# Kernel optimization log

Measured on AMD Instinct MI355X. Metric: run time of the kernel, lower is better.

## Reference

```python
import jax, jax.numpy as jnp
import numpy as np

NUM_MEL = 80
STACK_FRAMES = 4   # encoder.embed.right_context + 1
STRIDE = 4         # encoder.embed.subsampling_rate
N_SUB = 1          # n_subsequent
NCB = 1            # num_codebooks
EMB_DIM = 16
NUM_EMB = 8192
ENC_DIM = 512
B, T = 16, 2048
T_ENC = (T - STACK_FRAMES) // STRIDE + 1  # 512
EPS_LN = 1e-6


def setup_inputs() -> dict:
    key = jax.random.key(0)
    k = jax.random.split(key, 6)
    feats = jax.random.normal(k[0], (B, T, NUM_MEL), dtype=jnp.float32)
    feats_lengths = jax.random.randint(k[1], (B,), T // 2, T + 1, dtype=jnp.int32)
    encoder_out = jax.random.normal(k[2], (B, T_ENC, ENC_DIM), dtype=jnp.float32)
    in_dim = NUM_MEL * STRIDE
    lim = float(np.sqrt(6.0 / (in_dim + EMB_DIM * NCB)))  # xavier-uniform
    projection = jax.random.uniform(k[3], (in_dim, EMB_DIM * NCB), jnp.float32, -lim, lim)
    emb = jax.random.normal(k[4], (NUM_EMB, NCB, EMB_DIM), dtype=jnp.float32)
    embeddings = emb / (jnp.linalg.norm(emb, axis=-1, keepdims=True) + 1e-8)
    top_n_out = 0.02 * jax.random.normal(k[5], (N_SUB, NCB, ENC_DIM, NUM_EMB), dtype=jnp.float32)
    return {"feats": feats, "feats_lengths": feats_lengths, "encoder_out": encoder_out,
            "projection": projection, "embeddings": embeddings, "top_n_out": top_n_out}


def _stack_features(feats, lens):
    b, t, f = feats.shape
    n = (t - STACK_FRAMES) // STRIDE + 1
    idx = jnp.arange(n)[:, None] * STRIDE + jnp.arange(STACK_FRAMES)[None, :]  # [n, S]
    stack = feats[:, idx, :].reshape(b, n, STACK_FRAMES * f)                   # [B, n, S*F]
    mask = jnp.arange(t)[None, :] < lens[:, None]                              # [B, T]
    sub_mask = jnp.all(mask[:, idx], axis=-1)                                  # [B, n]
    mean = stack.mean(-1, keepdims=True)
    var = stack.var(-1, keepdims=True)
    stack = (stack - mean) * jax.lax.rsqrt(var + EPS_LN)  # LayerNorm, no affine
    return stack, sub_mask


def _nearest_idx(stack, projection, embeddings):
    x = stack @ projection                                         # [B, n, ncb*E]
    x = x / (jnp.linalg.norm(x, axis=-1, keepdims=True) + 1e-8)
    b, n, _ = x.shape
    v, ncb, e = embeddings.shape
    xf = x.reshape(b * n, ncb, e)
    dots = jnp.einsum('nce,vce->ncv', xf, embeddings)              # [N, ncb, V]
    x2 = jnp.sum(xf * xf, -1, keepdims=True)                       # [N, ncb, 1]
    e2 = jnp.sum(embeddings * embeddings, -1).T[None]              # [1, ncb, V]
    dist = x2 - 2.0 * dots + e2
    codes = jnp.argmin(dist, axis=-1)                              # [N, ncb]
    return codes.reshape(b, n, ncb)


def _forward(feats, feats_lengths, encoder_out, projection, embeddings, top_n_out):
    stack, stack_mask = _stack_features(feats, feats_lengths)
    target = _nearest_idx(stack, projection, embeddings)           # [B, n, ncb]
    tq = stack_mask.shape[1]
    # unfold(n_subsequent=1) -> [B, Tq, ns, ncb]
    target = target[:, :tq, None, :]
    # encoder output mask (subsampled lengths)
    t_enc = encoder_out.shape[1]
    out_mask = jnp.arange(t_enc)[None, :] < (feats_lengths // STRIDE)[:, None]
    logits = jnp.einsum('btd,scdv->bsctv', encoder_out, top_n_out)  # [B, ns, ncb, T', V]
    logits = logits[:, :, :, :tq, :][:, :, :, :-1, :]               # frames 0..Tq-2
    target = target[:, 1:]                                          # targets 1..Tq-1
    masks = (out_mask[:, :tq] & stack_mask)[:, 1:]                  # [B, Tq-1] bool
    mf = masks.astype(logits.dtype)
    logp = jax.nn.log_softmax(logits, axis=-1)
    tgt_bsct = jnp.transpose(target, (0, 2, 3, 1))                  # [B, ns, ncb, Tq-1]
    nll = -jnp.take_along_axis(logp, tgt_bsct[..., None], axis=-1)[..., 0]
    mfull = jnp.broadcast_to(mf[:, None, None, :], nll.shape)
    loss = (nll * mfull).sum() / mfull.sum()
    num_codes = mf.sum() * NCB
    pred = jnp.argmax(logits, axis=-1)                              # [B, ns, ncb, Tq-1]
    corr = (pred == tgt_bsct).astype(logits.dtype)
    codes_acc = (corr * mfull).sum() / num_codes
    masked_tgt = target * masks[:, :, None, None].astype(target.dtype)
    presence = jnp.zeros((NUM_EMB,), jnp.int32).at[masked_tgt.reshape(-1)].set(1)
    uniq_num_codes = presence.sum().astype(jnp.float32)
    return loss, codes_acc, num_codes, uniq_num_codes


def reference(feats, feats_lengths, encoder_out, projection, embeddings, top_n_out):
    return _forward(feats, feats_lengths, encoder_out, projection, embeddings, top_n_out)
```

## Files before the change

### kernel.cpp

```cpp
#include <hip/hip_runtime.h>
#include <math.h>

typedef __attribute__((ext_vector_type(4))) float f32x4;
typedef __attribute__((ext_vector_type(8))) short bf16x8;

#define NB 16
#define NT 2048
#define NMEL 80
#define NPOS 512
#define EDIM 16
#define NEMB 8192
#define ENCD 512
#define MROWS (NB*511)
#define MPAD 8192
#define NVT 64

__device__ __forceinline__ unsigned short f2bf(float x) {
    union { float f; unsigned u; } v; v.f = x;
    unsigned r = v.u + 0x7fffu + ((v.u >> 16) & 1u);
    return (unsigned short)(r >> 16);
}

__device__ __forceinline__ void gl_lds16(const void* gsrc, void* lds) {
    __builtin_amdgcn_global_load_lds(
        (const __attribute__((address_space(1))) unsigned int*)gsrc,
        (__attribute__((address_space(3))) unsigned int*)lds,
        16, 0, 0);
}

__global__ __launch_bounds__(256) void prep_kernel(
    const float* __restrict__ feats, const float* __restrict__ proj,
    const float* __restrict__ emb, const float* __restrict__ enc,
    const float* __restrict__ tno,
    unsigned short* __restrict__ ynB, unsigned short* __restrict__ embB,
    float* __restrict__ h2, int* __restrict__ presence,
    unsigned char* __restrict__ encF8, unsigned char* __restrict__ tnoF8)
{
    __shared__ float tileT[32][33];
    const int bid = blockIdx.x;
    const int tid = threadIdx.x;

    if (bid < 512) {
        const int lane = tid & 63;
        const int wave = tid >> 6;
        const int gbase = bid * 16 + wave * 4;
        if (bid < 32) presence[bid * 256 + tid] = 0;

        float yn[4][EDIM];
        #pragma unroll
        for (int pi = 0; pi < 4; ++pi) {
            const int g = gbase + pi;
            const int b = g >> 9;
            const int i = g & 511;
            float xv[5];
            float s = 0.f, sq = 0.f;
            #pragma unroll
            for (int qq = 0; qq < 5; ++qq) {
                const int d = lane + 64 * qq;
                const int j = d / 80, k = d - j * 80;
                const float v = feats[((b * NT) + (i * 4 + j)) * NMEL + k];
                xv[qq] = v; s += v; sq += v * v;
            }
            for (int m = 1; m < 64; m <<= 1) { s += __shfl_xor(s, m); sq += __shfl_xor(sq, m); }
            const float mean = s * (1.0f / 320.0f);
            const float var  = sq * (1.0f / 320.0f) - mean * mean;
            const float rstd = rsqrtf(var + 1e-6f);
            float acc[EDIM];
            #pragma unroll
            for (int e = 0; e < EDIM; ++e) acc[e] = 0.f;
            #pragma unroll
            for (int qq = 0; qq < 5; ++qq) {
                const int d = lane + 64 * qq;
                const float xn = (xv[qq] - mean) * rstd;
                #pragma unroll
                for (int e = 0; e < EDIM; ++e) acc[e] += xn * proj[d * EDIM + e];
            }
            for (int m = 1; m < 64; m <<= 1) {
                #pragma unroll
                for (int e = 0; e < EDIM; ++e) acc[e] += __shfl_xor(acc[e], m);
            }
            float nsq = 0.f;
            #pragma unroll
            for (int e = 0; e < EDIM; ++e) nsq += acc[e] * acc[e];
            const float inv = 1.0f / (sqrtf(nsq) + 1e-8f);
            #pragma unroll
            for (int e = 0; e < EDIM; ++e) yn[pi][e] = acc[e] * inv;
        }
        #pragma unroll
        for (int pi = 0; pi < 4; ++pi) {
            if (lane == pi) {
                unsigned short* dst = &ynB[(size_t)(gbase + pi) * 32];
                #pragma unroll
                for (int e = 0; e < EDIM; ++e) dst[e] = f2bf(yn[pi][e]);
                #pragma unroll
                for (int e = EDIM; e < 32; ++e) dst[e] = 0;
            }
        }
    } else if (bid < 1024) {
        const int bid2 = bid - 512;
        const int lane = tid & 63;
        #pragma unroll
        for (int pass = 0; pass < 4; ++pass) {
            const int m = bid2 * 16 + pass * 4 + (tid >> 6);
            const int d = lane * 8;
            uint2 o = make_uint2(0u, 0u);
            if (m < MROWS) {
                const int b = m / 511, t = m - b * 511;
                const float4 f0 = *(const float4*)&enc[((size_t)(b * 512 + t)) * ENCD + d];
                const float4 f1 = *(const float4*)&enc[((size_t)(b * 512 + t)) * ENCD + d + 4];
                int w0 = __builtin_amdgcn_cvt_pk_fp8_f32(f0.x, f0.y, 0, false);
                w0     = __builtin_amdgcn_cvt_pk_fp8_f32(f0.z, f0.w, w0, true);
                int w1 = __builtin_amdgcn_cvt_pk_fp8_f32(f1.x, f1.y, 0, false);
                w1     = __builtin_amdgcn_cvt_pk_fp8_f32(f1.z, f1.w, w1, true);
                o.x = (unsigned)w0; o.y = (unsigned)w1;
            }
            *(uint2*)&encF8[(size_t)m * ENCD + d] = o;
        }
    } else if (bid < 2048) {
        const int bid2 = bid - 1024;
        const int tx = tid & 31, ty = tid >> 5;
        const int np = tid >> 3, kc = tid & 7;
        #pragma unroll
        for (int it = 0; it < 4; ++it) {
            const int tile = bid2 * 4 + it;
            const int n0 = (tile & 255) * 32;
            const int k0 = (tile >> 8) * 32;
            __syncthreads();
            #pragma unroll
            for (int i = 0; i < 4; ++i)
                tileT[ty + 8 * i][tx] = tno[(size_t)(k0 + ty + 8 * i) * NEMB + n0 + tx];
            __syncthreads();
            const float t0 = 16.0f * tileT[kc * 4 + 0][np];
            const float t1 = 16.0f * tileT[kc * 4 + 1][np];
            const float t2 = 16.0f * tileT[kc * 4 + 2][np];
            const float t3 = 16.0f * tileT[kc * 4 + 3][np];
            int w = __builtin_amdgcn_cvt_pk_fp8_f32(t0, t1, 0, false);
            w     = __builtin_amdgcn_cvt_pk_fp8_f32(t2, t3, w, true);
            ((unsigned*)tnoF8)[(size_t)(n0 + np) * (ENCD / 4) + (k0 >> 2) + kc] = (unsigned)w;
        }
    } else {
        const int row = (bid - 2048) * 256 + tid;
        const float* ep = &emb[(size_t)row * EDIM];
        const float4 e0 = *(const float4*)&ep[0];
        const float4 e1 = *(const float4*)&ep[4];
        const float4 e2v = *(const float4*)&ep[8];
        const float4 e3 = *(const float4*)&ep[12];
        const float e2 = e0.x*e0.x + e0.y*e0.y + e0.z*e0.z + e0.w*e0.w
                       + e1.x*e1.x + e1.y*e1.y + e1.z*e1.z + e1.w*e1.w
                       + e2v.x*e2v.x + e2v.y*e2v.y + e2v.z*e2v.z + e2v.w*e2v.w
                       + e3.x*e3.x + e3.y*e3.y + e3.z*e3.z + e3.w*e3.w;
        h2[row] = 0.5f * e2;
        unsigned short* dst = &embB[(size_t)row * 32];
        dst[0]  = f2bf(e0.x); dst[1]  = f2bf(e0.y); dst[2]  = f2bf(e0.z); dst[3]  = f2bf(e0.w);
        dst[4]  = f2bf(e1.x); dst[5]  = f2bf(e1.y); dst[6]  = f2bf(e1.z); dst[7]  = f2bf(e1.w);
        dst[8]  = f2bf(e2v.x); dst[9]  = f2bf(e2v.y); dst[10] = f2bf(e2v.z); dst[11] = f2bf(e2v.w);
        dst[12] = f2bf(e3.x); dst[13] = f2bf(e3.y); dst[14] = f2bf(e3.z); dst[15] = f2bf(e3.w);
        #pragma unroll
        for (int e = EDIM; e < 32; ++e) dst[e] = 0;
    }
}

__global__ __launch_bounds__(256) void codes_mfma(
    const unsigned short* __restrict__ ynB, const unsigned short* __restrict__ embB,
    const float* __restrict__ h2,
    float* __restrict__ pscore, int* __restrict__ pcidx)
{
    const int tid = threadIdx.x;
    const int lane = tid & 63;
    const int wave = tid >> 6;
    const int pgrp  = blockIdx.x >> 2;
    const int chunk = blockIdx.x & 3;
    const int p0 = pgrp * 64 + wave * 16;
    const int l15 = lane & 15, q = lane >> 4;

    const bf16x8 a = *(const bf16x8*)&ynB[(size_t)(p0 + l15) * 32 + q * 8];

    float mn[4]; int mi[4];
    #pragma unroll
    for (int r = 0; r < 4; ++r) { mn[r] = INFINITY; mi[r] = 0x7fffffff; }

    const int e0 = chunk * 2048;
    #pragma unroll 4
    for (int g = 0; g < 128; ++g) {
        const int eidx = e0 + g * 16 + l15;
        const bf16x8 b = *(const bf16x8*)&embB[(size_t)eidx * 32 + q * 8];
        const float hv = h2[eidx];
        f32x4 d = __builtin_amdgcn_mfma_f32_16x16x32_bf16(a, b, (f32x4){0.f, 0.f, 0.f, 0.f}, 0, 0, 0);
        #pragma unroll
        for (int r = 0; r < 4; ++r) {
            const float sc = hv - d[r];
            if (sc < mn[r]) { mn[r] = sc; mi[r] = eidx; }
        }
    }
    #pragma unroll
    for (int m = 1; m < 16; m <<= 1) {
        #pragma unroll
        for (int r = 0; r < 4; ++r) {
            const float ov = __shfl_xor(mn[r], m);
            const int   oi = __shfl_xor(mi[r], m);
            if (ov < mn[r] || (ov == mn[r] && oi < mi[r])) { mn[r] = ov; mi[r] = oi; }
        }
    }
    if (l15 == 0) {
        #pragma unroll
        for (int r = 0; r < 4; ++r) {
            pscore[chunk * MPAD + p0 + q * 4 + r] = mn[r];
            pcidx [chunk * MPAD + p0 + q * 4 + r] = mi[r];
        }
    }
}

__global__ __launch_bounds__(256) void codes_merge(
    const float* __restrict__ pscore, const int* __restrict__ pcidx,
    int* __restrict__ codes)
{
    const int g = blockIdx.x * 256 + threadIdx.x;
    float m = INFINITY; int mi = 0x7fffffff;
    #pragma unroll
    for (int c = 0; c < 4; ++c) {
        const float s = pscore[c * MPAD + g];
        const int  ix = pcidx [c * MPAD + g];
        if (s < m || (s == m && ix < mi)) { m = s; mi = ix; }
    }
    codes[g] = mi;
}

__global__ __launch_bounds__(256, 5) void logits_mfma(
    const unsigned char* __restrict__ encF8, const unsigned char* __restrict__ tnoF8,
    const int* __restrict__ codes,
    float* __restrict__ pm, float* __restrict__ ps, int* __restrict__ pidx,
    float* __restrict__ tgtlog)
{
    __shared__ __align__(16) unsigned char As3[3][128 * 32];
    __shared__ __align__(16) unsigned char Bs3[3][128 * 32];
    __shared__ float redM[2][128];
    __shared__ float redS[2][128];
    __shared__ int   redI[2][128];

    const int tid  = threadIdx.x;
    const int lane = tid & 63;
    const int wave = tid >> 6;
    const int wr = wave >> 1, wc = wave & 1;

    const int bid = blockIdx.x;
    const int xcd = bid & 7;
    const int idx = bid >> 3;
    const int mt  = xcd * 8 + (idx & 7);
    const int vt  = idx >> 3;
    const int m0 = mt * 128, n0 = vt * 128;

    const int srow = lane >> 1;
    const int gcB  = ((lane & 1) ^ ((lane >> 3) & 1)) * 16;
    const size_t abase0 = (size_t)(m0 + wave * 32 + srow) * ENCD + gcB;
    const size_t bbase0 = (size_t)(n0 + wave * 32 + srow) * ENCD + gcB;

#define STAGE(t, buf)                                                                        \
    {                                                                                        \
        const int k0s = (t) * 32;                                                            \
        gl_lds16(encF8 + abase0 + k0s, &As3[buf][(wave * 32) * 32]);                         \
        gl_lds16(tnoF8 + bbase0 + k0s, &Bs3[buf][(wave * 32) * 32]);                         \
    }

    f32x4 acc[4][4];
    #pragma unroll
    for (int i = 0; i < 4; ++i)
        #pragma unroll
        for (int j = 0; j < 4; ++j)
            acc[i][j] = (f32x4){0.f, 0.f, 0.f, 0.f};

    const int l15 = lane & 15, q = lane >> 4;
    const int rsw = (l15 >> 2) & 1;
    const int co  = (((q >> 1) ^ rsw) * 16) + (q & 1) * 8;

    STAGE(0, 0);
    STAGE(1, 1);

    #pragma unroll
    for (int t = 0; t < 16; ++t) {
        if (t < 15) { asm volatile("s_waitcnt vmcnt(2)" ::: "memory"); }
        else        { asm volatile("s_waitcnt vmcnt(0)" ::: "memory"); }
        __builtin_amdgcn_s_barrier();
        __builtin_amdgcn_sched_barrier(0);
        if (t + 2 < 16) {
            const int nb = (t + 2) % 3;
            STAGE(t + 2, nb);
        }
        const unsigned char* Ab = As3[t % 3];
        const unsigned char* Bb = Bs3[t % 3];
        long a[4], b[4];
        #pragma unroll
        for (int mi = 0; mi < 4; ++mi)
            a[mi] = *(const long*)&Ab[(wr * 64 + mi * 16 + l15) * 32 + co];
        #pragma unroll
        for (int ni = 0; ni < 4; ++ni)
            b[ni] = *(const long*)&Bb[(wc * 64 + ni * 16 + l15) * 32 + co];
        __builtin_amdgcn_s_setprio(1);
        #pragma unroll
        for (int mi = 0; mi < 4; ++mi)
            #pragma unroll
            for (int ni = 0; ni < 4; ++ni)
                acc[mi][ni] = __builtin_amdgcn_mfma_f32_16x16x32_fp8_fp8(a[mi], b[ni], acc[mi][ni], 0, 0, 0);
        __builtin_amdgcn_s_setprio(0);
    }
#undef STAGE

    #pragma unroll
    for (int mi = 0; mi < 4; ++mi)
        #pragma unroll
        for (int ni = 0; ni < 4; ++ni)
            acc[mi][ni] *= 0.0625f;

    #pragma unroll
    for (int mi = 0; mi < 4; ++mi) {
        #pragma unroll
        for (int r = 0; r < 4; ++r) {
            const int rl = wr * 64 + mi * 16 + q * 4 + r;
            float lm = -INFINITY; int li = 0;
            #pragma unroll
            for (int ni = 0; ni < 4; ++ni) {
                const float v = acc[mi][ni][r];
                const int col = wc * 64 + ni * 16 + l15;
                if (v > lm) { lm = v; li = col; }
            }
            #pragma unroll
            for (int mk = 8; mk >= 1; mk >>= 1) {
                const float ov = __shfl_xor(lm, mk);
                const int   oi = __shfl_xor(li, mk);
                if (ov > lm || (ov == lm && oi < li)) { lm = ov; li = oi; }
            }
            float le = 0.f;
            #pragma unroll
            for (int ni = 0; ni < 4; ++ni) le += __expf(acc[mi][ni][r] - lm);
            #pragma unroll
            for (int mk = 8; mk >= 1; mk >>= 1) le += __shfl_xor(le, mk);

            if (l15 == 0) { redM[wc][rl] = lm; redS[wc][rl] = le; redI[wc][rl] = li; }

            const int mg = m0 + rl;
            if (mg < MROWS) {
                const int bb = mg / 511, tt = mg - bb * 511;
                const int tv = codes[bb * NPOS + tt + 1];
                const int rel = tv - n0 - wc * 64;
                #pragma unroll
                for (int ni = 0; ni < 4; ++ni) {
                    if (rel >= ni * 16 && rel < ni * 16 + 16 && (rel & 15) == l15)
                        tgtlog[mg] = acc[mi][ni][r];
                }
            }
        }
    }
    __syncthreads();
    if (tid < 128) {
        const int rl = tid;
        const int mg = m0 + rl;
        if (mg < MROWS) {
            const float mA = redM[0][rl], mB = redM[1][rl];
            const int   iA = redI[0][rl], iB = redI[1][rl];
            float gm; int gi;
            if (mB > mA || (mB == mA && iB + 64 < iA)) { gm = mB; gi = 64 + iB; } else { gm = mA; gi = iA; }
            const float S = redS[0][rl] * __expf(mA - gm) + redS[1][rl] * __expf(mB - gm);
            pm[(size_t)vt * MPAD + mg]   = gm;
            ps[(size_t)vt * MPAD + mg]   = S;
            pidx[(size_t)vt * MPAD + mg] = n0 + gi;
        }
    }
}

__global__ __launch_bounds__(256) void combine_kernel(
    const float* __restrict__ pm, const float* __restrict__ ps,
    const int* __restrict__ pidx, const float* __restrict__ tgtlog,
    const int* __restrict__ codes, const int* __restrict__ lens,
    float* __restrict__ rnll, float* __restrict__ rcorr, float* __restrict__ rmf,
    int* __restrict__ presence)
{
    const int g = blockIdx.x * 256 + threadIdx.x;
    if (g >= MROWS) return;
    float gm = -INFINITY; int gi = 0;
    #pragma unroll 8
    for (int nt = 0; nt < NVT; ++nt) {
        const float v = pm[(size_t)nt * MPAD + g];
        if (v > gm) { gm = v; gi = pidx[(size_t)nt * MPAD + g]; }
    }
    float S = 0.f;
    #pragma unroll 8
    for (int nt = 0; nt < NVT; ++nt) S += ps[(size_t)nt * MPAD + g] * __expf(pm[(size_t)nt * MPAD + g] - gm);
    const float lse = gm + logf(S);
    const int b = g / 511, t = g - b * 511;
    const int tv = codes[b * NPOS + t + 1];
    const float nll = lse - tgtlog[g];
    const int L = lens[b];
    const int s = t + 1;
    const bool mf = (s < (L / 4)) && (4 * s + 3 < L);
    rnll[g]  = mf ? nll : 0.f;
    rcorr[g] = (mf && gi == tv) ? 1.f : 0.f;
    rmf[g]   = mf ? 1.f : 0.f;
    if (mf) presence[tv] = 1;
}

__global__ __launch_bounds__(256) void finalize_kernel(
    const float* __restrict__ rnll, const float* __restrict__ rcorr,
    const float* __restrict__ rmf, const int* __restrict__ presence,
    float* __restrict__ out)
{
    __shared__ float sh0[256], sh1[256], sh2[256];
    __shared__ int shp[256];
    const int tid = threadIdx.x;
    float sn = 0.f, sc = 0.f, sm = 0.f; int pp = 0;
    for (int g = tid; g < MROWS; g += 256) { sn += rnll[g]; sc += rcorr[g]; sm += rmf[g]; }
    for (int v = tid; v < NEMB; v += 256) pp += presence[v];
    sh0[tid] = sn; sh1[tid] = sc; sh2[tid] = sm; shp[tid] = pp;
    __syncthreads();
    for (int s = 128; s > 0; s >>= 1) {
        if (tid < s) { sh0[tid] += sh0[tid + s]; sh1[tid] += sh1[tid + s]; sh2[tid] += sh2[tid + s]; shp[tid] += shp[tid + s]; }
        __syncthreads();
    }
    if (tid == 0) {
        const float Sm = sh2[0];
        out[0] = sh0[0] / Sm;
        out[1] = sh1[0] / Sm;
        out[2] = Sm;
        out[3] = (float)shp[0];
    }
}

extern "C" void kernel_launch(void* const* d_in, const int* in_sizes, int n_in,
                              void* d_out, int out_size, void* d_ws, size_t ws_size,
                              hipStream_t stream) {
    const float* feats = (const float*)d_in[0];
    const int*   lens  = (const int*)d_in[1];
    const float* enc   = (const float*)d_in[2];
    const float* proj  = (const float*)d_in[3];
    const float* emb   = (const float*)d_in[4];
    const float* tno   = (const float*)d_in[5];
    float* out = (float*)d_out;

    int* codes          = (int*)d_ws;
    int* presence       = codes + MPAD;
    float* pm           = (float*)(presence + MPAD);
    float* ps           = pm + (size_t)NVT * MPAD;
    int* pidx           = (int*)(ps + (size_t)NVT * MPAD);
    float* tgtlog       = (float*)(pidx + (size_t)NVT * MPAD);
    float* rnll         = tgtlog + MPAD;
    float* rcorr        = rnll + MPAD;
    float* rmf          = rcorr + MPAD;
    float* pscore       = rmf + MPAD;
    int*   pcidx        = (int*)(pscore + 4 * MPAD);
    float* h2           = (float*)(pcidx + 4 * MPAD);
    unsigned short* ynB  = (unsigned short*)(h2 + MPAD);
    unsigned short* embB = ynB + (size_t)MPAD * 32;
    unsigned char* encF8 = (unsigned char*)(embB + (size_t)MPAD * 32);
    unsigned char* tnoF8 = encF8 + (size_t)MPAD * ENCD;

    hipLaunchKernelGGL(prep_kernel, dim3(2080), dim3(256), 0, stream,
                       feats, proj, emb, enc, tno, ynB, embB, h2, presence, encF8, tnoF8);
    hipLaunchKernelGGL(codes_mfma, dim3(512), dim3(256), 0, stream, ynB, embB, h2, pscore, pcidx);
    hipLaunchKernelGGL(codes_merge, dim3(32), dim3(256), 0, stream, pscore, pcidx, codes);
    hipLaunchKernelGGL(logits_mfma, dim3(64 * 64), dim3(256), 0, stream, encF8, tnoF8, codes, pm, ps, pidx, tgtlog);
    hipLaunchKernelGGL(combine_kernel, dim3((MROWS + 255) / 256), dim3(256), 0, stream,
                       pm, ps, pidx, tgtlog, codes, lens, rnll, rcorr, rmf, presence);
    hipLaunchKernelGGL(finalize_kernel, dim3(1), dim3(256), 0, stream, rnll, rcorr, rmf, presence, out);
}
```

Baseline: 212.4 us.

## Fuse finalize into combine via last-block atomic reduction; lower logits occupancy hint

Merges the single-block finalize kernel into combine_kernel. Each block reduces its rows' nll/correct/mask sums in shared memory and writes per-block partials, and the last block to arrive (found with an atomic counter reset in prep_kernel) sums the partials and the presence array and writes the outputs. This removes one kernel launch and the per-row intermediate buffers. Separately, the logits_mfma launch bound changes from 5 to 4 minimum blocks per CU, which gives the compiler more registers at the cost of possible occupancy.

```diff
diff --git a/kernel.cpp b/kernel.cpp
--- a/kernel.cpp
+++ b/kernel.cpp
@@ -33,7 +33,7 @@
     const float* __restrict__ emb, const float* __restrict__ enc,
     const float* __restrict__ tno,
     unsigned short* __restrict__ ynB, unsigned short* __restrict__ embB,
-    float* __restrict__ h2, int* __restrict__ presence,
+    float* __restrict__ h2, int* __restrict__ presence, int* __restrict__ sctrl,
     unsigned char* __restrict__ encF8, unsigned char* __restrict__ tnoF8)
 {
     __shared__ float tileT[32][33];
@@ -45,6 +45,7 @@
         const int wave = tid >> 6;
         const int gbase = bid * 16 + wave * 4;
         if (bid < 32) presence[bid * 256 + tid] = 0;
+        if (bid == 32 && tid < 160) sctrl[tid] = 0;
 
         float yn[4][EDIM];
         #pragma unroll
@@ -225,7 +226,7 @@
     codes[g] = mi;
 }
 
-__global__ __launch_bounds__(256, 5) void logits_mfma(
+__global__ __launch_bounds__(256, 4) void logits_mfma(
     const unsigned char* __restrict__ encF8, const unsigned char* __restrict__ tnoF8,
     const int* __restrict__ codes,
     float* __restrict__ pm, float* __restrict__ ps, int* __restrict__ pidx,
@@ -370,55 +371,76 @@
     const float* __restrict__ pm, const float* __restrict__ ps,
     const int* __restrict__ pidx, const float* __restrict__ tgtlog,
     const int* __restrict__ codes, const int* __restrict__ lens,
-    float* __restrict__ rnll, float* __restrict__ rcorr, float* __restrict__ rmf,
-    int* __restrict__ presence)
-{
-    const int g = blockIdx.x * 256 + threadIdx.x;
-    if (g >= MROWS) return;
-    float gm = -INFINITY; int gi = 0;
-    #pragma unroll 8
-    for (int nt = 0; nt < NVT; ++nt) {
-        const float v = pm[(size_t)nt * MPAD + g];
-        if (v > gm) { gm = v; gi = pidx[(size_t)nt * MPAD + g]; }
-    }
-    float S = 0.f;
-    #pragma unroll 8
-    for (int nt = 0; nt < NVT; ++nt) S += ps[(size_t)nt * MPAD + g] * __expf(pm[(size_t)nt * MPAD + g] - gm);
-    const float lse = gm + logf(S);
-    const int b = g / 511, t = g - b * 511;
-    const int tv = codes[b * NPOS + t + 1];
-    const float nll = lse - tgtlog[g];
-    const int L = lens[b];
-    const int s = t + 1;
-    const bool mf = (s < (L / 4)) && (4 * s + 3 < L);
-    rnll[g]  = mf ? nll : 0.f;
-    rcorr[g] = (mf && gi == tv) ? 1.f : 0.f;
-    rmf[g]   = mf ? 1.f : 0.f;
-    if (mf) presence[tv] = 1;
-}
-
-__global__ __launch_bounds__(256) void finalize_kernel(
-    const float* __restrict__ rnll, const float* __restrict__ rcorr,
-    const float* __restrict__ rmf, const int* __restrict__ presence,
+    int* __restrict__ presence, int* __restrict__ sctrl,
     float* __restrict__ out)
 {
-    __shared__ float sh0[256], sh1[256], sh2[256];
+    float* partials = (float*)(sctrl + 64);
+    const int tid = threadIdx.x;
+    const int g = blockIdx.x * 256 + tid;
+    float nll = 0.f, corr = 0.f, mfv = 0.f;
+    if (g < MROWS) {
+        float gm = -INFINITY; int gi = 0;
+        #pragma unroll 8
+        for (int nt = 0; nt < NVT; ++nt) {
+            const float v = pm[(size_t)nt * MPAD + g];
+            if (v > gm) { gm = v; gi = pidx[(size_t)nt * MPAD + g]; }
+        }
+        float S = 0.f;
+        #pragma unroll 8
+        for (int nt = 0; nt < NVT; ++nt) S += ps[(size_t)nt * MPAD + g] * __expf(pm[(size_t)nt * MPAD + g] - gm);
+        const float lse = gm + logf(S);
+        const int b = g / 511, t = g - b * 511;
+        const int tv = codes[b * NPOS + t + 1];
+        const int L = lens[b];
+        const int s = t + 1;
+        const bool mf = (s < (L / 4)) && (4 * s + 3 < L);
+        if (mf) {
+            nll = lse - tgtlog[g];
+            corr = (gi == tv) ? 1.f : 0.f;
+            mfv = 1.f;
+            presence[tv] = 1;
+        }
+    }
+    __shared__ float s0[256], s1[256], s2[256];
     __shared__ int shp[256];
-    const int tid = threadIdx.x;
-    float sn = 0.f, sc = 0.f, sm = 0.f; int pp = 0;
-    for (int g = tid; g < MROWS; g += 256) { sn += rnll[g]; sc += rcorr[g]; sm += rmf[g]; }
+    __shared__ int isLast;
+    s0[tid] = nll; s1[tid] = corr; s2[tid] = mfv;
+    __syncthreads();
+    for (int st = 128; st > 0; st >>= 1) {
+        if (tid < st) { s0[tid] += s0[tid + st]; s1[tid] += s1[tid + st]; s2[tid] += s2[tid + st]; }
+        __syncthreads();
+    }
+    if (tid == 0) {
+        partials[blockIdx.x * 3 + 0] = s0[0];
+        partials[blockIdx.x * 3 + 1] = s1[0];
+        partials[blockIdx.x * 3 + 2] = s2[0];
+        __threadfence();
+        isLast = (atomicAdd(&sctrl[0], 1) == 31);
+    }
+    __syncthreads();
+    if (!isLast) return;
+    __threadfence();
+
+    float tn = 0.f, tc = 0.f, tm = 0.f;
+    if (tid == 0) {
+        for (int i = 0; i < 32; ++i) {
+            tn += partials[i * 3 + 0];
+            tc += partials[i * 3 + 1];
+            tm += partials[i * 3 + 2];
+        }
+    }
+    int pp = 0;
     for (int v = tid; v < NEMB; v += 256) pp += presence[v];
-    sh0[tid] = sn; sh1[tid] = sc; sh2[tid] = sm; shp[tid] = pp;
+    shp[tid] = pp;
     __syncthreads();
-    for (int s = 128; s > 0; s >>= 1) {
-        if (tid < s) { sh0[tid] += sh0[tid + s]; sh1[tid] += sh1[tid + s]; sh2[tid] += sh2[tid + s]; shp[tid] += shp[tid + s]; }
+    for (int st = 128; st > 0; st >>= 1) {
+        if (tid < st) shp[tid] += shp[tid + st];
         __syncthreads();
     }
     if (tid == 0) {
-        const float Sm = sh2[0];
-        out[0] = sh0[0] / Sm;
-        out[1] = sh1[0] / Sm;
-        out[2] = Sm;
+        out[0] = tn / tm;
+        out[1] = tc / tm;
+        out[2] = tm;
         out[3] = (float)shp[0];
     }
 }
@@ -440,23 +462,20 @@
     float* ps           = pm + (size_t)NVT * MPAD;
     int* pidx           = (int*)(ps + (size_t)NVT * MPAD);
     float* tgtlog       = (float*)(pidx + (size_t)NVT * MPAD);
-    float* rnll         = tgtlog + MPAD;
-    float* rcorr        = rnll + MPAD;
-    float* rmf          = rcorr + MPAD;
-    float* pscore       = rmf + MPAD;
+    float* pscore       = tgtlog + MPAD;
     int*   pcidx        = (int*)(pscore + 4 * MPAD);
     float* h2           = (float*)(pcidx + 4 * MPAD);
-    unsigned short* ynB  = (unsigned short*)(h2 + MPAD);
+    int*   sctrl        = (int*)(h2 + MPAD);
+    unsigned short* ynB  = (unsigned short*)(sctrl + 160);
     unsigned short* embB = ynB + (size_t)MPAD * 32;
     unsigned char* encF8 = (unsigned char*)(embB + (size_t)MPAD * 32);
     unsigned char* tnoF8 = encF8 + (size_t)MPAD * ENCD;
 
     hipLaunchKernelGGL(prep_kernel, dim3(2080), dim3(256), 0, stream,
-                       feats, proj, emb, enc, tno, ynB, embB, h2, presence, encF8, tnoF8);
+                       feats, proj, emb, enc, tno, ynB, embB, h2, presence, sctrl, encF8, tnoF8);
     hipLaunchKernelGGL(codes_mfma, dim3(512), dim3(256), 0, stream, ynB, embB, h2, pscore, pcidx);
     hipLaunchKernelGGL(codes_merge, dim3(32), dim3(256), 0, stream, pscore, pcidx, codes);
     hipLaunchKernelGGL(logits_mfma, dim3(64 * 64), dim3(256), 0, stream, encF8, tnoF8, codes, pm, ps, pidx, tgtlog);
-    hipLaunchKernelGGL(combine_kernel, dim3((MROWS + 255) / 256), dim3(256), 0, stream,
-                       pm, ps, pidx, tgtlog, codes, lens, rnll, rcorr, rmf, presence);
-    hipLaunchKernelGGL(finalize_kernel, dim3(1), dim3(256), 0, stream, rnll, rcorr, rmf, presence, out);
-}
+    hipLaunchKernelGGL(combine_kernel, dim3(32), dim3(256), 0, stream,
+                       pm, ps, pidx, tgtlog, codes, lens, presence, sctrl, out);
+}
```

Result: no change. 210.5 us (-0.9%).
